# Kernel tuning notes

Measured on AMD Instinct MI355X. Metric: run time of the kernel, lower is better.

## Reference

```python
import jax, jax.numpy as jnp
import numpy as np

LATENT_DIM = 128
KQ_DIM = 32
B, N, K = 8, 16384, 16


def setup_inputs() -> dict:
    key = jax.random.key(0)
    k1, k2, k3, k4, k5, k6 = jax.random.split(key, 6)
    features = jax.random.normal(k1, (B, N, LATENT_DIM), dtype=jnp.float32)
    ks_w = jax.random.normal(k2, (KQ_DIM, LATENT_DIM), dtype=jnp.float32) * (LATENT_DIM ** -0.5)
    ks_b = jax.random.normal(k3, (KQ_DIM,), dtype=jnp.float32) * 0.01
    qs_w = jax.random.normal(k4, (KQ_DIM, LATENT_DIM), dtype=jnp.float32) * (LATENT_DIM ** -0.5)
    qs_b = jax.random.normal(k5, (KQ_DIM,), dtype=jnp.float32) * 0.01
    indices = jax.random.randint(k6, (3, B, N, K), 0, N, dtype=jnp.int64)
    return {"features": features, "ks_w": ks_w, "ks_b": ks_b,
            "qs_w": qs_w, "qs_b": qs_b, "indices": indices}


def reference(features, ks_w, ks_b, qs_w, qs_b, indices):
    # features: [B, N, latent_dim]; indices: [3, B, N, K]
    b, n, _ = features.shape
    k = indices.shape[-1]
    # Linear projections (torch Linear: x @ W^T + b)
    flatten_ks = jnp.einsum('bnl,dl->bnd', features, ks_w) + ks_b  # [B,N,D]
    flatten_qs = jnp.einsum('bnl,dl->bnd', features, qs_w) + qs_b  # [B,N,D]
    d = flatten_ks.shape[-1]
    # gather along node dim N using index channels 1 (x) and 2 (y)
    x_idx = indices[1].reshape(b, n * k)  # [B, N*K]
    y_idx = indices[2].reshape(b, n * k)
    x_features = jnp.take_along_axis(flatten_ks, x_idx[..., None], axis=1).reshape(b, n, k, d)
    y_features = jnp.take_along_axis(flatten_qs, y_idx[..., None], axis=1).reshape(b, n, k, d)
    # scaled dot-product affinity
    logits = jnp.sum(x_features * y_features, axis=-1) * (d ** -0.5)  # [B,N,K]
    return logits
```

## Files before the change

### kernel.cpp

```cpp
#include <hip/hip_runtime.h>

#define BATCH   8
#define NNODES  16384
#define KNBR    16
#define LATENT  128
#define DOUT    32
#define NROWS   (BATCH * NNODES)

typedef __attribute__((ext_vector_type(8))) short short8;
typedef __attribute__((ext_vector_type(4))) float floatx4;

__device__ __forceinline__ unsigned short f2bf(float f) {
    unsigned u = __float_as_uint(f);
    u += 0x7fff + ((u >> 16) & 1);
    return (unsigned short)(u >> 16);
}

__device__ __forceinline__ float dot2bf(unsigned a, unsigned b) {
    float alo = __uint_as_float(a << 16);
    float ahi = __uint_as_float(a & 0xffff0000u);
    float blo = __uint_as_float(b << 16);
    float bhi = __uint_as_float(b & 0xffff0000u);
    return alo * blo + ahi * bhi;
}

__device__ __forceinline__ void gload_lds16(const float* g, void* l) {
    __builtin_amdgcn_global_load_lds(
        (const __attribute__((address_space(1))) void*)g,
        (__attribute__((address_space(3))) void*)l,
        16, 0, 0);
}

#define BPAD 136

__global__ __launch_bounds__(256) void proj_kernel(
    const float* __restrict__ feats,
    const float* __restrict__ kw, const float* __restrict__ kb,
    const float* __restrict__ qw, const float* __restrict__ qb,
    unsigned short* __restrict__ tkb, unsigned short* __restrict__ tqb)
{
    __shared__ __align__(16) unsigned char A_raw[128 * 256];
    __shared__ unsigned short B_lds[64 * BPAD];
    __shared__ float bias_lds[64];

    const int tid  = threadIdx.x;
    const int lane = tid & 63;
    const int w    = tid >> 6;
    const long long blk_row = (long long)blockIdx.x * 128;

    {
        const float4* kw4 = (const float4*)kw;
        const float4* qw4 = (const float4*)qw;
#pragma unroll
        for (int i = 0; i < 8; ++i) {
            const int linear = i * 256 + tid;
            const int row = linear >> 5;
            const int c4  = linear & 31;
            const float4 v = (row < 32) ? kw4[row * 32 + c4] : qw4[(row - 32) * 32 + c4];
            unsigned lo = f2bf(v.x) | ((unsigned)f2bf(v.y) << 16);
            unsigned hi = f2bf(v.z) | ((unsigned)f2bf(v.w) << 16);
            *(uint2*)&B_lds[row * BPAD + c4 * 4] = make_uint2(lo, hi);
        }
        if (tid < 64) bias_lds[tid] = (tid < 32) ? kb[tid] : qb[tid - 32];
    }

    const int m = lane & 15;
    const int q = lane >> 4;

    floatx4 acc[2][4];
#pragma unroll
    for (int rt = 0; rt < 2; ++rt)
#pragma unroll
        for (int ct = 0; ct < 4; ++ct) acc[rt][ct] = (floatx4){0.f, 0.f, 0.f, 0.f};

    for (int ch = 0; ch < 2; ++ch) {
        if (ch) __syncthreads();

#pragma unroll
        for (int i = 0; i < 8; ++i) {
            const int L  = i * 4096 + tid * 16;
            const int r  = L >> 8;
            const int c0 = (((L & 255) ^ ((r & 7) << 4)) >> 2);
            gload_lds16(feats + (blk_row + r) * 128 + ch * 64 + c0, A_raw + L);
        }
        __syncthreads();

#pragma unroll
        for (int ks = 0; ks < 2; ++ks) {
            const int kg = ch * 64 + ks * 32 + q * 8;
            short8 bf[4];
#pragma unroll
            for (int ct = 0; ct < 4; ++ct)
                bf[ct] = *(const short8*)&B_lds[(ct * 16 + m) * BPAD + kg];
#pragma unroll
            for (int rt = 0; rt < 2; ++rt) {
                const int rloc = w * 32 + rt * 16 + m;
                const int b0   = rloc * 256 + ks * 128 + q * 32;
                const int p0   = b0 ^ ((rloc & 7) << 4);
                const float4 a0 = *(const float4*)(A_raw + p0);
                const float4 a1 = *(const float4*)(A_raw + (p0 ^ 16));
                union { short8 s; unsigned u[4]; } af;
                af.u[0] = f2bf(a0.x) | ((unsigned)f2bf(a0.y) << 16);
                af.u[1] = f2bf(a0.z) | ((unsigned)f2bf(a0.w) << 16);
                af.u[2] = f2bf(a1.x) | ((unsigned)f2bf(a1.y) << 16);
                af.u[3] = f2bf(a1.z) | ((unsigned)f2bf(a1.w) << 16);
#pragma unroll
                for (int ct = 0; ct < 4; ++ct)
                    acc[rt][ct] = __builtin_amdgcn_mfma_f32_16x16x32_bf16(af.s, bf[ct], acc[rt][ct], 0, 0, 0);
            }
        }
    }

#pragma unroll
    for (int rt = 0; rt < 2; ++rt) {
#pragma unroll
        for (int reg = 0; reg < 4; ++reg) {
            const long long row = blk_row + w * 32 + rt * 16 + q * 4 + reg;
#pragma unroll
            for (int ct = 0; ct < 4; ++ct) {
                const float val = acc[rt][ct][reg] + bias_lds[ct * 16 + m];
                if (ct < 2) tkb[row * DOUT + ct * 16 + m]       = f2bf(val);
                else        tqb[row * DOUT + (ct - 2) * 16 + m] = f2bf(val);
            }
        }
    }
}

__global__ __launch_bounds__(256) void gather_dot_kernel(
    const unsigned short* __restrict__ tkb, const unsigned short* __restrict__ tqb,
    const int* __restrict__ idx, float* __restrict__ out)
{
    const long long NK  = (long long)NNODES * KNBR;
    const long long BNK = NK * BATCH;

    const int b   = blockIdx.x & 7;
    const int blk = blockIdx.x >> 3;
    const int grp = threadIdx.x >> 2;
    const int j   = threadIdx.x & 3;

    const uint4* tb_k = (const uint4*)(tkb + (long long)b * NNODES * DOUT);
    const uint4* tb_q = (const uint4*)(tqb + (long long)b * NNODES * DOUT);

#pragma unroll
    for (int p = 0; p < 4; ++p) {
        const long long local = (long long)blk * 256 + p * 64 + grp;
        const long long o     = (long long)b * NK + local;

        const int xi = __builtin_nontemporal_load(&idx[BNK + o]);
        const int yi = __builtin_nontemporal_load(&idx[2 * BNK + o]);

        const uint4 x = tb_k[(long long)xi * 4 + j];
        const uint4 y = tb_q[(long long)yi * 4 + j];
        float s = dot2bf(x.x, y.x) + dot2bf(x.y, y.y)
                + dot2bf(x.z, y.z) + dot2bf(x.w, y.w);
        s += __shfl_xor(s, 1);
        s += __shfl_xor(s, 2);
        if (j == 0)
            __builtin_nontemporal_store(s * 0.17677669529663687f, &out[o]);
    }
}

extern "C" void kernel_launch(void* const* d_in, const int* in_sizes, int n_in,
                              void* d_out, int out_size, void* d_ws, size_t ws_size,
                              hipStream_t stream)
{
    const float* feats = (const float*)d_in[0];
    const float* kw    = (const float*)d_in[1];
    const float* kb    = (const float*)d_in[2];
    const float* qw    = (const float*)d_in[3];
    const float* qb    = (const float*)d_in[4];
    const int*   idx   = (const int*)d_in[5];
    float*       out   = (float*)d_out;

    unsigned short* tkb = (unsigned short*)d_ws;
    unsigned short* tqb = tkb + (long long)NROWS * DOUT;

    proj_kernel<<<NROWS / 128, 256, 0, stream>>>(feats, kw, kb, qw, qb, tkb, tqb);
    gather_dot_kernel<<<(int)((long long)BATCH * NNODES * KNBR / 256), 256, 0, stream>>>(
        tkb, tqb, idx, out);
}
```

Before: 146.6 us.

## Fuse projection and gather-dot into one persistent cooperative kernel with grid sync

Merges the projection GEMM and the gather-dot kernel into a single persistent cooperative kernel. Blocks loop over 64-row tiles, with the full 128-wide K held in LDS, then sync the whole grid before the gather phase. Each block is pinned to one batch so its gathers hit that batch's slice of the projected tables. This removes a kernel launch and the weight reload per tile, but adds a grid-wide barrier and caps occupancy at three blocks per CU.

```diff
diff --git a/kernel.cpp b/kernel.cpp
--- a/kernel.cpp
+++ b/kernel.cpp
@@ -1,4 +1,7 @@
 #include <hip/hip_runtime.h>
+#include <hip/hip_cooperative_groups.h>
+
+namespace cg = cooperative_groups;
 
 #define BATCH   8
 #define NNODES  16384
@@ -33,20 +36,22 @@
 
 #define BPAD 136
 
-__global__ __launch_bounds__(256) void proj_kernel(
+__global__ __launch_bounds__(256) void fused_kernel(
     const float* __restrict__ feats,
     const float* __restrict__ kw, const float* __restrict__ kb,
     const float* __restrict__ qw, const float* __restrict__ qb,
+    const int* __restrict__ idx, float* __restrict__ out,
     unsigned short* __restrict__ tkb, unsigned short* __restrict__ tqb)
 {
-    __shared__ __align__(16) unsigned char A_raw[128 * 256];
+    __shared__ __align__(16) unsigned char A_raw[64 * 512];
     __shared__ unsigned short B_lds[64 * BPAD];
     __shared__ float bias_lds[64];
 
     const int tid  = threadIdx.x;
     const int lane = tid & 63;
     const int w    = tid >> 6;
-    const long long blk_row = (long long)blockIdx.x * 128;
+    const int bid  = blockIdx.x;
+    const int nb   = gridDim.x;
 
     {
         const float4* kw4 = (const float4*)kw;
@@ -67,96 +72,87 @@
     const int m = lane & 15;
     const int q = lane >> 4;
 
-    floatx4 acc[2][4];
-#pragma unroll
-    for (int rt = 0; rt < 2; ++rt)
-#pragma unroll
-        for (int ct = 0; ct < 4; ++ct) acc[rt][ct] = (floatx4){0.f, 0.f, 0.f, 0.f};
-
-    for (int ch = 0; ch < 2; ++ch) {
-        if (ch) __syncthreads();
+    const int bgrp = nb >> 3;
+    const int bat  = bid & 7;
+    for (int u = bid >> 3; u < 256; u += bgrp) {
+        const long long blk_row = ((long long)bat * 256 + u) * 64;
+        __syncthreads();
 
 #pragma unroll
         for (int i = 0; i < 8; ++i) {
             const int L  = i * 4096 + tid * 16;
-            const int r  = L >> 8;
-            const int c0 = (((L & 255) ^ ((r & 7) << 4)) >> 2);
-            gload_lds16(feats + (blk_row + r) * 128 + ch * 64 + c0, A_raw + L);
+            const int r  = L >> 9;
+            const int c0 = ((L & 511) ^ ((r & 7) << 4)) >> 2;
+            gload_lds16(feats + (blk_row + r) * 128 + c0, A_raw + L);
         }
         __syncthreads();
 
+        floatx4 acc[4];
 #pragma unroll
-        for (int ks = 0; ks < 2; ++ks) {
-            const int kg = ch * 64 + ks * 32 + q * 8;
-            short8 bf[4];
+        for (int ct = 0; ct < 4; ++ct) acc[ct] = (floatx4){0.f, 0.f, 0.f, 0.f};
+
+        const int rloc = w * 16 + m;
+        const int sw   = (rloc & 7) << 4;
 #pragma unroll
-            for (int ct = 0; ct < 4; ++ct)
-                bf[ct] = *(const short8*)&B_lds[(ct * 16 + m) * BPAD + kg];
+        for (int ks = 0; ks < 4; ++ks) {
+            const int b0 = rloc * 512 + ks * 128 + q * 32;
+            const int p0 = b0 ^ sw;
+            const float4 a0 = *(const float4*)(A_raw + p0);
+            const float4 a1 = *(const float4*)(A_raw + (p0 ^ 16));
+            union { short8 s; unsigned uu[4]; } af;
+            af.uu[0] = f2bf(a0.x) | ((unsigned)f2bf(a0.y) << 16);
+            af.uu[1] = f2bf(a0.z) | ((unsigned)f2bf(a0.w) << 16);
+            af.uu[2] = f2bf(a1.x) | ((unsigned)f2bf(a1.y) << 16);
+            af.uu[3] = f2bf(a1.z) | ((unsigned)f2bf(a1.w) << 16);
+            const int kg = ks * 32 + q * 8;
 #pragma unroll
-            for (int rt = 0; rt < 2; ++rt) {
-                const int rloc = w * 32 + rt * 16 + m;
-                const int b0   = rloc * 256 + ks * 128 + q * 32;
-                const int p0   = b0 ^ ((rloc & 7) << 4);
-                const float4 a0 = *(const float4*)(A_raw + p0);
-                const float4 a1 = *(const float4*)(A_raw + (p0 ^ 16));
-                union { short8 s; unsigned u[4]; } af;
-                af.u[0] = f2bf(a0.x) | ((unsigned)f2bf(a0.y) << 16);
-                af.u[1] = f2bf(a0.z) | ((unsigned)f2bf(a0.w) << 16);
-                af.u[2] = f2bf(a1.x) | ((unsigned)f2bf(a1.y) << 16);
-                af.u[3] = f2bf(a1.z) | ((unsigned)f2bf(a1.w) << 16);
-#pragma unroll
-                for (int ct = 0; ct < 4; ++ct)
-                    acc[rt][ct] = __builtin_amdgcn_mfma_f32_16x16x32_bf16(af.s, bf[ct], acc[rt][ct], 0, 0, 0);
+            for (int ct = 0; ct < 4; ++ct) {
+                const short8 bf = *(const short8*)&B_lds[(ct * 16 + m) * BPAD + kg];
+                acc[ct] = __builtin_amdgcn_mfma_f32_16x16x32_bf16(af.s, bf, acc[ct], 0, 0, 0);
             }
         }
-    }
 
 #pragma unroll
-    for (int rt = 0; rt < 2; ++rt) {
-#pragma unroll
         for (int reg = 0; reg < 4; ++reg) {
-            const long long row = blk_row + w * 32 + rt * 16 + q * 4 + reg;
+            const long long row = blk_row + w * 16 + q * 4 + reg;
 #pragma unroll
             for (int ct = 0; ct < 4; ++ct) {
-                const float val = acc[rt][ct][reg] + bias_lds[ct * 16 + m];
+                const float val = acc[ct][reg] + bias_lds[ct * 16 + m];
                 if (ct < 2) tkb[row * DOUT + ct * 16 + m]       = f2bf(val);
                 else        tqb[row * DOUT + (ct - 2) * 16 + m] = f2bf(val);
             }
         }
     }
-}
 
-__global__ __launch_bounds__(256) void gather_dot_kernel(
-    const unsigned short* __restrict__ tkb, const unsigned short* __restrict__ tqb,
-    const int* __restrict__ idx, float* __restrict__ out)
-{
+    cg::this_grid().sync();
+
     const long long NK  = (long long)NNODES * KNBR;
     const long long BNK = NK * BATCH;
+    const int grp = tid >> 2;
+    const int j   = tid & 3;
 
-    const int b   = blockIdx.x & 7;
-    const int blk = blockIdx.x >> 3;
-    const int grp = threadIdx.x >> 2;
-    const int j   = threadIdx.x & 3;
+    const uint4* tb_k = (const uint4*)(tkb + (long long)bat * NNODES * DOUT);
+    const uint4* tb_q = (const uint4*)(tqb + (long long)bat * NNODES * DOUT);
 
-    const uint4* tb_k = (const uint4*)(tkb + (long long)b * NNODES * DOUT);
-    const uint4* tb_q = (const uint4*)(tqb + (long long)b * NNODES * DOUT);
+    for (int g = bid; g < 8192; g += nb) {
+        const int blk = g >> 3;
+#pragma unroll
+        for (int p = 0; p < 4; ++p) {
+            const long long local = (long long)blk * 256 + p * 64 + grp;
+            const long long o     = (long long)bat * NK + local;
 
-#pragma unroll
-    for (int p = 0; p < 4; ++p) {
-        const long long local = (long long)blk * 256 + p * 64 + grp;
-        const long long o     = (long long)b * NK + local;
+            const int xi = __builtin_nontemporal_load(&idx[BNK + o]);
+            const int yi = __builtin_nontemporal_load(&idx[2 * BNK + o]);
 
-        const int xi = __builtin_nontemporal_load(&idx[BNK + o]);
-        const int yi = __builtin_nontemporal_load(&idx[2 * BNK + o]);
-
-        const uint4 x = tb_k[(long long)xi * 4 + j];
-        const uint4 y = tb_q[(long long)yi * 4 + j];
-        float s = dot2bf(x.x, y.x) + dot2bf(x.y, y.y)
-                + dot2bf(x.z, y.z) + dot2bf(x.w, y.w);
-        s += __shfl_xor(s, 1);
-        s += __shfl_xor(s, 2);
-        if (j == 0)
-            __builtin_nontemporal_store(s * 0.17677669529663687f, &out[o]);
+            const uint4 x = tb_k[(long long)xi * 4 + j];
+            const uint4 y = tb_q[(long long)yi * 4 + j];
+            float s = dot2bf(x.x, y.x) + dot2bf(x.y, y.y)
+                    + dot2bf(x.z, y.z) + dot2bf(x.w, y.w);
+            s += __shfl_xor(s, 1);
+            s += __shfl_xor(s, 2);
+            if (j == 0)
+                __builtin_nontemporal_store(s * 0.17677669529663687f, &out[o]);
+        }
     }
 }
 
@@ -175,7 +171,13 @@
     unsigned short* tkb = (unsigned short*)d_ws;
     unsigned short* tqb = tkb + (long long)NROWS * DOUT;
 
-    proj_kernel<<<NROWS / 128, 256, 0, stream>>>(feats, kw, kb, qw, qb, tkb, tqb);
-    gather_dot_kernel<<<(int)((long long)BATCH * NNODES * KNBR / 256), 256, 0, stream>>>(
-        tkb, tqb, idx, out);
+    int occ = 0;
+    if (hipOccupancyMaxActiveBlocksPerMultiprocessor(&occ, fused_kernel, 256, 0)
+            != hipSuccess || occ < 1) occ = 2;
+    if (occ > 3) occ = 3;
+    const int nb = occ * 256;
+
+    void* args[] = {(void*)&feats, (void*)&kw, (void*)&kb, (void*)&qw, (void*)&qb,
+                    (void*)&idx, (void*)&out, (void*)&tkb, (void*)&tqb};
+    hipLaunchCooperativeKernel(fused_kernel, dim3(nb), dim3(256), args, 0, stream);
 }
```

Result: slower. 269.2 us (+83.6%).

## Use one thread per gathered pair and interleave projection blocks across batches

Applied to the files above, without the earlier changes.

The gather-dot kernel now assigns each thread a whole (node, neighbor) pair. Each thread loads the full 64-byte bf16 rows for x and y and reduces locally, which removes the 4-lane split and the cross-lane shuffles. Index loads and output stores become fully coalesced per thread, and the grid shrinks fourfold. The projection kernel remaps block IDs so consecutive blocks cover different batches, presumably to spread L2/channel placement or match the gather's batch interleaving. The risk is that per-thread 64-byte scattered loads may be less efficiently coalesced than the 4-lane cooperative 16-byte loads.

```diff
diff --git a/kernel.cpp b/kernel.cpp
--- a/kernel.cpp
+++ b/kernel.cpp
@@ -46,7 +46,9 @@
     const int tid  = threadIdx.x;
     const int lane = tid & 63;
     const int w    = tid >> 6;
-    const long long blk_row = (long long)blockIdx.x * 128;
+    const int bat  = blockIdx.x & 7;
+    const int u    = blockIdx.x >> 3;
+    const long long blk_row = (long long)bat * NNODES + (long long)u * 128;
 
     {
         const float4* kw4 = (const float4*)kw;
@@ -99,11 +101,11 @@
                 const int p0   = b0 ^ ((rloc & 7) << 4);
                 const float4 a0 = *(const float4*)(A_raw + p0);
                 const float4 a1 = *(const float4*)(A_raw + (p0 ^ 16));
-                union { short8 s; unsigned u[4]; } af;
-                af.u[0] = f2bf(a0.x) | ((unsigned)f2bf(a0.y) << 16);
-                af.u[1] = f2bf(a0.z) | ((unsigned)f2bf(a0.w) << 16);
-                af.u[2] = f2bf(a1.x) | ((unsigned)f2bf(a1.y) << 16);
-                af.u[3] = f2bf(a1.z) | ((unsigned)f2bf(a1.w) << 16);
+                union { short8 s; unsigned uu[4]; } af;
+                af.uu[0] = f2bf(a0.x) | ((unsigned)f2bf(a0.y) << 16);
+                af.uu[1] = f2bf(a0.z) | ((unsigned)f2bf(a0.w) << 16);
+                af.uu[2] = f2bf(a1.x) | ((unsigned)f2bf(a1.y) << 16);
+                af.uu[3] = f2bf(a1.z) | ((unsigned)f2bf(a1.w) << 16);
 #pragma unroll
                 for (int ct = 0; ct < 4; ++ct)
                     acc[rt][ct] = __builtin_amdgcn_mfma_f32_16x16x32_bf16(af.s, bf[ct], acc[rt][ct], 0, 0, 0);
@@ -133,30 +135,36 @@
     const long long NK  = (long long)NNODES * KNBR;
     const long long BNK = NK * BATCH;
 
-    const int b   = blockIdx.x & 7;
+    const int bat = blockIdx.x & 7;
     const int blk = blockIdx.x >> 3;
-    const int grp = threadIdx.x >> 2;
-    const int j   = threadIdx.x & 3;
+    const int tid = threadIdx.x;
 
-    const uint4* tb_k = (const uint4*)(tkb + (long long)b * NNODES * DOUT);
-    const uint4* tb_q = (const uint4*)(tqb + (long long)b * NNODES * DOUT);
+    const uint4* tb_k = (const uint4*)(tkb + (long long)bat * NNODES * DOUT);
+    const uint4* tb_q = (const uint4*)(tqb + (long long)bat * NNODES * DOUT);
 
 #pragma unroll
     for (int p = 0; p < 4; ++p) {
-        const long long local = (long long)blk * 256 + p * 64 + grp;
-        const long long o     = (long long)b * NK + local;
+        const long long local = (long long)blk * 1024 + p * 256 + tid;
+        const long long o     = (long long)bat * NK + local;
 
         const int xi = __builtin_nontemporal_load(&idx[BNK + o]);
         const int yi = __builtin_nontemporal_load(&idx[2 * BNK + o]);
 
-        const uint4 x = tb_k[(long long)xi * 4 + j];
-        const uint4 y = tb_q[(long long)yi * 4 + j];
-        float s = dot2bf(x.x, y.x) + dot2bf(x.y, y.y)
-                + dot2bf(x.z, y.z) + dot2bf(x.w, y.w);
-        s += __shfl_xor(s, 1);
-        s += __shfl_xor(s, 2);
-        if (j == 0)
-            __builtin_nontemporal_store(s * 0.17677669529663687f, &out[o]);
+        const uint4* xr = tb_k + (long long)xi * 4;
+        const uint4* yr = tb_q + (long long)yi * 4;
+        const uint4 x0 = xr[0], x1 = xr[1], x2 = xr[2], x3 = xr[3];
+        const uint4 y0 = yr[0], y1 = yr[1], y2 = yr[2], y3 = yr[3];
+
+        float s = dot2bf(x0.x, y0.x) + dot2bf(x0.y, y0.y)
+                + dot2bf(x0.z, y0.z) + dot2bf(x0.w, y0.w)
+                + dot2bf(x1.x, y1.x) + dot2bf(x1.y, y1.y)
+                + dot2bf(x1.z, y1.z) + dot2bf(x1.w, y1.w)
+                + dot2bf(x2.x, y2.x) + dot2bf(x2.y, y2.y)
+                + dot2bf(x2.z, y2.z) + dot2bf(x2.w, y2.w)
+                + dot2bf(x3.x, y3.x) + dot2bf(x3.y, y3.y)
+                + dot2bf(x3.z, y3.z) + dot2bf(x3.w, y3.w);
+
+        __builtin_nontemporal_store(s * 0.17677669529663687f, &out[o]);
     }
 }
 
@@ -176,6 +184,6 @@
     unsigned short* tqb = tkb + (long long)NROWS * DOUT;
 
     proj_kernel<<<NROWS / 128, 256, 0, stream>>>(feats, kw, kb, qw, qb, tkb, tqb);
-    gather_dot_kernel<<<(int)((long long)BATCH * NNODES * KNBR / 256), 256, 0, stream>>>(
+    gather_dot_kernel<<<(int)((long long)BATCH * NNODES * KNBR / 1024), 256, 0, stream>>>(
         tkb, tqb, idx, out);
 }
```

After: 163.9 us. 1.12x slower.
